# Performance work log

Hardware: AMD Instinct MI355X
Metric: run time of the kernel (lower is better)

Reference implementation:

```python
import jax, jax.numpy as jnp
import numpy as np

M = 12          # persons per frame
K = 2           # partition channels from conv1da (1024 = 2*512)
D = 512         # GCN channel dim / LSTM hidden
C_IN = 4096     # backbone feature dim
NUM_CLASSES = 8


def setup_inputs() -> dict:
    key = jax.random.key(0)
    ks = jax.random.split(key, 8)
    N, T = 16, 32
    NT = N * T
    base_out = jax.random.normal(ks[0], (NT, M, C_IN), dtype=jnp.float32)
    dist = jax.random.uniform(ks[1], (N, T, 3, K, M, M), dtype=jnp.float32)
    # conv1da: Conv1d(4096 -> 1024, k=1, bias=False) == matmul with [1024, 4096]
    w_a = jax.random.normal(ks[2], (K * D, C_IN), dtype=jnp.float32) * 0.02
    # LSTM(512, 512, 1): torch gate order i, f, g, o
    s = 1.0 / np.sqrt(D)
    w_ih = jax.random.uniform(ks[3], (4 * D, D), minval=-s, maxval=s, dtype=jnp.float32)
    w_hh = jax.random.uniform(ks[4], (4 * D, D), minval=-s, maxval=s, dtype=jnp.float32)
    b_ih = jax.random.uniform(ks[5], (4 * D,), minval=-s, maxval=s, dtype=jnp.float32)
    b_hh = jax.random.uniform(ks[6], (4 * D,), minval=-s, maxval=s, dtype=jnp.float32)
    # gclassifier: Linear(512 -> num_classes)
    w_cls = jax.random.normal(ks[7], (NUM_CLASSES, D), dtype=jnp.float32) * 0.01
    b_cls = jnp.zeros((NUM_CLASSES,), dtype=jnp.float32)
    return {"base_out": base_out, "dist": dist, "w_a": w_a,
            "w_ih": w_ih, "w_hh": w_hh, "b_ih": b_ih, "b_hh": b_hh,
            "w_cls": w_cls, "b_cls": b_cls, "n_videos": N}


def reference(base_out, dist, w_a, w_ih, w_hh, b_ih, b_hh, w_cls, b_cls, n_videos):
    NT = base_out.shape[0]
    N = n_videos
    T = NT // N
    # conv1da (1x1 conv, no bias): [NT, M, 4096] -> [NT, K*D, M] -> [NT, K, D, M]
    node1 = jnp.einsum('nmc,oc->nom', base_out, w_a).reshape(NT, K, D, M)
    # fused three-way adjacency aggregation: node1a + node1b + node1c
    A = (dist[:, :, 2] + dist[:, :, 1] + dist[:, :, 0]).reshape(NT, K, M, M)
    node = jnp.einsum('nkcv,nkvw->ncw', node1, A)  # [NT, D, M]
    node = jax.nn.relu(node)
    # AdaptiveAvgPool1d(1) over the M persons
    pooled = node.mean(axis=2)                      # [NT, D]
    seq = pooled.reshape(N, T, D)
    # torch nn.LSTM default batch_first=False: iterates over axis 0 (N), batch=T
    def step(carry, x_t):
        h, c = carry
        g = x_t @ w_ih.T + b_ih + h @ w_hh.T + b_hh  # [T, 4D]
        i, f, gg, o = jnp.split(g, 4, axis=-1)
        c = jax.nn.sigmoid(f) * c + jax.nn.sigmoid(i) * jnp.tanh(gg)
        h = jax.nn.sigmoid(o) * jnp.tanh(c)
        return (h, c), h
    h0 = jnp.zeros((T, D), dtype=seq.dtype)
    c0 = jnp.zeros((T, D), dtype=seq.dtype)
    _, hs = jax.lax.scan(step, (h0, c0), seq)       # [N, T, D]
    last = hs[:, -1, :]                              # video_feat[:, -1, :]
    return last @ w_cls.T + b_cls                    # [N, num_classes]
```

## Files before the change

### kernel.cpp

```cpp
#include <hip/hip_runtime.h>
#include <math.h>

#define MM 12
#define KK 2
#define DD 512
#define CIN 4096
#define NCLS 8
#define NV 16
#define TT 32

typedef unsigned long long u64;
typedef __attribute__((ext_vector_type(8))) __bf16 bf16x8;
typedef __attribute__((ext_vector_type(4))) float f32x4;

#define PART_F   0
#define POOLED_F 786432
#define TAGA_F   794624
#define TAGB_F   794880
#define PART_KS_STRIDE (192 * 1024)

#define MFMA_BF16(A, B, C) __builtin_amdgcn_mfma_f32_16x16x32_bf16((A), (B), (C), 0, 0, 0)

__global__ __launch_bounds__(256, 1) void k_fused(
    const float* __restrict__ base_out, const float* __restrict__ dist,
    const float* __restrict__ w_a, const float* __restrict__ w_ih,
    const float* __restrict__ w_hh, const float* __restrict__ b_ih,
    const float* __restrict__ b_hh, const float* __restrict__ w_cls,
    const float* __restrict__ b_cls,
    float* __restrict__ part, float* __restrict__ pooled,
    unsigned* __restrict__ tagA, unsigned* __restrict__ tagB,
    u64* __restrict__ slots, float* __restrict__ out)
{
  const int wg = blockIdx.x;
  const int tid = threadIdx.x;

  __shared__ __align__(16) unsigned short Ah[16 * 40], Al[16 * 40];
  __shared__ __align__(16) unsigned short Bh[192 * 40], Bl[192 * 40];
  __shared__ __align__(16) float whh_s[16][516];
  __shared__ __align__(16) float wih_s[16][516];
  __shared__ __align__(16) float pooled_s[16][520];
  __shared__ float gx_s[16][20];
  __shared__ __align__(16) float h_s[DD];
  __shared__ float dot_s[16];
  __shared__ float Asum_s[KK * MM * MM];

  {
    const int ks = wg >> 6, ot = wg & 63;
    const int cc0 = ks * 1024;
    const int wave = tid >> 6, lane = tid & 63;
    const int jf0 = wave * 3;

    const int sq = tid & 7;
    const int sr = tid >> 3;
    unsigned boff[6];
#pragma unroll
    for (int rep = 0; rep < 6; ++rep) {
      const int j = sr + 32 * rep;
      const int n = j / 12, m = j - n * 12;
      boff[rep] = (unsigned)(((n * TT + 31) * MM + m) * CIN + cc0 + sq * 4);
    }
    const bool aact = tid < 128;
    unsigned aoff = aact ? (unsigned)((ot * 16 + (tid >> 3)) * CIN + cc0 + sq * 4) : 0u;

    f32x4 acc0 = {0.f, 0.f, 0.f, 0.f}, acc1 = acc0, acc2 = acc0;

    float4 pa, pb[6];
    if (aact) pa = *(const float4*)&w_a[aoff];
#pragma unroll
    for (int rep = 0; rep < 6; ++rep) pb[rep] = *(const float4*)&base_out[boff[rep]];

    for (int st = 0; st < 32; ++st) {
      __syncthreads();
      if (aact) {
        const int idx = (tid >> 3) * 40 + sq * 4;
        unsigned ux = __float_as_uint(pa.x), uy = __float_as_uint(pa.y);
        unsigned uz = __float_as_uint(pa.z), uw = __float_as_uint(pa.w);
        *(uint2*)&Ah[idx] = make_uint2((ux >> 16) | (uy & 0xFFFF0000u),
                                       (uz >> 16) | (uw & 0xFFFF0000u));
        unsigned lx = __float_as_uint(pa.x - __uint_as_float(ux & 0xFFFF0000u));
        unsigned ly = __float_as_uint(pa.y - __uint_as_float(uy & 0xFFFF0000u));
        unsigned lz = __float_as_uint(pa.z - __uint_as_float(uz & 0xFFFF0000u));
        unsigned lw = __float_as_uint(pa.w - __uint_as_float(uw & 0xFFFF0000u));
        *(uint2*)&Al[idx] = make_uint2((lx >> 16) | (ly & 0xFFFF0000u),
                                       (lz >> 16) | (lw & 0xFFFF0000u));
      }
#pragma unroll
      for (int rep = 0; rep < 6; ++rep) {
        const int idx = (sr + 32 * rep) * 40 + sq * 4;
        unsigned ux = __float_as_uint(pb[rep].x), uy = __float_as_uint(pb[rep].y);
        unsigned uz = __float_as_uint(pb[rep].z), uw = __float_as_uint(pb[rep].w);
        *(uint2*)&Bh[idx] = make_uint2((ux >> 16) | (uy & 0xFFFF0000u),
                                       (uz >> 16) | (uw & 0xFFFF0000u));
        unsigned lx = __float_as_uint(pb[rep].x - __uint_as_float(ux & 0xFFFF0000u));
        unsigned ly = __float_as_uint(pb[rep].y - __uint_as_float(uy & 0xFFFF0000u));
        unsigned lz = __float_as_uint(pb[rep].z - __uint_as_float(uz & 0xFFFF0000u));
        unsigned lw = __float_as_uint(pb[rep].w - __uint_as_float(uw & 0xFFFF0000u));
        *(uint2*)&Bl[idx] = make_uint2((lx >> 16) | (ly & 0xFFFF0000u),
                                       (lz >> 16) | (lw & 0xFFFF0000u));
      }
      __syncthreads();
      if (st < 31) {
        aoff += 32;
        if (aact) pa = *(const float4*)&w_a[aoff];
#pragma unroll
        for (int rep = 0; rep < 6; ++rep) {
          boff[rep] += 32;
          pb[rep] = *(const float4*)&base_out[boff[rep]];
        }
      }
      const int koff = (lane >> 4) * 8;
      const int fra = (lane & 15) * 40 + koff;
      bf16x8 oh = *(const bf16x8*)&Ah[fra];
      bf16x8 ol = *(const bf16x8*)&Al[fra];
      {
        const int r0 = ((jf0 + 0) * 16 + (lane & 15)) * 40 + koff;
        bf16x8 jh = *(const bf16x8*)&Bh[r0], jl = *(const bf16x8*)&Bl[r0];
        acc0 = MFMA_BF16(jh, oh, acc0);
        acc0 = MFMA_BF16(jh, ol, acc0);
        acc0 = MFMA_BF16(jl, oh, acc0);
      }
      {
        const int r1 = ((jf0 + 1) * 16 + (lane & 15)) * 40 + koff;
        bf16x8 jh = *(const bf16x8*)&Bh[r1], jl = *(const bf16x8*)&Bl[r1];
        acc1 = MFMA_BF16(jh, oh, acc1);
        acc1 = MFMA_BF16(jh, ol, acc1);
        acc1 = MFMA_BF16(jl, oh, acc1);
      }
      {
        const int r2 = ((jf0 + 2) * 16 + (lane & 15)) * 40 + koff;
        bf16x8 jh = *(const bf16x8*)&Bh[r2], jl = *(const bf16x8*)&Bl[r2];
        acc2 = MFMA_BF16(jh, oh, acc2);
        acc2 = MFMA_BF16(jh, ol, acc2);
        acc2 = MFMA_BF16(jl, oh, acc2);
      }
    }
    const int o = ot * 16 + (lane & 15);
    const int jr = (lane >> 4) * 4;
#pragma unroll
    for (int r = 0; r < 4; ++r) {
      part[((size_t)ks * 192 + (jf0 + 0) * 16 + jr + r) * 1024 + o] = acc0[r];
      part[((size_t)ks * 192 + (jf0 + 1) * 16 + jr + r) * 1024 + o] = acc1[r];
      part[((size_t)ks * 192 + (jf0 + 2) * 16 + jr + r) * 1024 + o] = acc2[r];
    }
    __syncthreads();
    if (tid == 0)
      __hip_atomic_store(&tagA[wg], 1u, __ATOMIC_RELEASE, __HIP_MEMORY_SCOPE_AGENT);
  }

  if (wg < 128) {
    for (int f = tid; f < 16 * DD; f += 256) {
      const int rl = f >> 9, col = f & 511;
      const int row = (rl >> 2) * DD + wg * 4 + (rl & 3);
      whh_s[rl][col] = w_hh[(size_t)row * DD + col];
      wih_s[rl][col] = w_ih[(size_t)row * DD + col];
    }
  }

  while (__hip_atomic_load(&tagA[tid], __ATOMIC_RELAXED, __HIP_MEMORY_SCOPE_AGENT) != 1u) {}
  __syncthreads();
  (void)__hip_atomic_load(&tagA[0], __ATOMIC_ACQUIRE, __HIP_MEMORY_SCOPE_AGENT);

  {
    const int n = wg >> 4, cb = (wg & 15) * 32;
    const unsigned dbase = (unsigned)((n * TT + 31) * (3 * KK * MM * MM));
    for (int f = tid; f < KK * MM * MM; f += 256)
      Asum_s[f] = dist[dbase + f] + dist[dbase + KK * MM * MM + f]
                + dist[dbase + 2 * KK * MM * MM + f];
    __syncthreads();
    if (tid < 32) {
      const int c = cb + tid;
      float nd[KK][MM];
#pragma unroll
      for (int k = 0; k < KK; ++k)
#pragma unroll
        for (int v = 0; v < MM; ++v) {
          const size_t off = (size_t)(n * MM + v) * 1024 + k * DD + c;
          nd[k][v] = part[off] + part[off + PART_KS_STRIDE]
                   + part[off + 2 * PART_KS_STRIDE] + part[off + 3 * PART_KS_STRIDE];
        }
      float accm = 0.f;
#pragma unroll
      for (int w = 0; w < MM; ++w) {
        float sw = 0.f;
#pragma unroll
        for (int k = 0; k < KK; ++k)
#pragma unroll
          for (int v = 0; v < MM; ++v) sw += nd[k][v] * Asum_s[(k * MM + v) * MM + w];
        accm += fmaxf(sw, 0.f);
      }
      pooled[n * DD + c] = accm * (1.f / 12.f);
    }
    __syncthreads();
    if (tid == 0)
      __hip_atomic_store(&tagB[wg], 1u, __ATOMIC_RELEASE, __HIP_MEMORY_SCOPE_AGENT);
  }
  if (wg >= 128) return;

  while (__hip_atomic_load(&tagB[tid], __ATOMIC_RELAXED, __HIP_MEMORY_SCOPE_AGENT) != 1u) {}
  __syncthreads();
  (void)__hip_atomic_load(&tagB[0], __ATOMIC_ACQUIRE, __HIP_MEMORY_SCOPE_AGENT);

  for (int f = tid; f < NV * DD; f += 256) pooled_s[f >> 9][f & 511] = pooled[f];
  __syncthreads();
  {
    const int rl = tid & 15, n = tid >> 4;
    const float4* wr = (const float4*)&wih_s[rl][0];
    const float4* pv = (const float4*)&pooled_s[n][0];
    float a = 0.f;
#pragma unroll 8
    for (int q = 0; q < DD / 4; ++q) {
      float4 x = wr[q], y = pv[q];
      a += x.x * y.x + x.y * y.y + x.z * y.z + x.w * y.w;
    }
    const int row = (rl >> 2) * DD + wg * 4 + (rl & 3);
    gx_s[n][rl] = a + b_ih[row] + b_hh[row];
  }
  __syncthreads();

  {
    float c_reg = 0.f;
    const int r = tid >> 4;
    const int lj = tid & 15;

    for (int s = 0; s < NV; ++s) {
      if (s == 0) {
        h_s[tid] = 0.f; h_s[tid + 256] = 0.f;
      } else {
        const u64* slot = slots + ((size_t)(wg & 7) * NV + (s - 1)) * DD;
        u64 v0 = __hip_atomic_load(&slot[tid], __ATOMIC_RELAXED, __HIP_MEMORY_SCOPE_AGENT);
        u64 v1 = __hip_atomic_load(&slot[tid + 256], __ATOMIC_RELAXED, __HIP_MEMORY_SCOPE_AGENT);
        while ((unsigned)v0 != (unsigned)s)
          v0 = __hip_atomic_load(&slot[tid], __ATOMIC_RELAXED, __HIP_MEMORY_SCOPE_AGENT);
        while ((unsigned)v1 != (unsigned)s)
          v1 = __hip_atomic_load(&slot[tid + 256], __ATOMIC_RELAXED, __HIP_MEMORY_SCOPE_AGENT);
        h_s[tid] = __uint_as_float((unsigned)(v0 >> 32));
        h_s[tid + 256] = __uint_as_float((unsigned)(v1 >> 32));
      }
      __syncthreads();

      float p = 0.f;
      const float4* wrow = (const float4*)&whh_s[r][0];
      const float4* hv4 = (const float4*)h_s;
#pragma unroll
      for (int q = 0; q < 8; ++q) {
        float4 wv = wrow[lj + 16 * q];
        float4 hv = hv4[lj + 16 * q];
        p += wv.x * hv.x + wv.y * hv.y + wv.z * hv.z + wv.w * hv.w;
      }
#pragma unroll
      for (int off = 8; off; off >>= 1) p += __shfl_down(p, off, 16);
      if (lj == 0) dot_s[r] = p;
      __syncthreads();

      u64 pack = 0;
      if (tid < 4) {
        const float pi = gx_s[s][tid]      + dot_s[tid];
        const float pf = gx_s[s][4 + tid]  + dot_s[4 + tid];
        const float pg = gx_s[s][8 + tid]  + dot_s[8 + tid];
        const float po = gx_s[s][12 + tid] + dot_s[12 + tid];
        const float si = 1.f / (1.f + expf(-pi));
        const float sf = 1.f / (1.f + expf(-pf));
        const float so = 1.f / (1.f + expf(-po));
        c_reg = sf * c_reg + si * tanhf(pg);
        const float hn = so * tanhf(c_reg);
        pack = ((u64)__float_as_uint(hn) << 32) | (u64)(unsigned)(s + 1);
      }
      if (tid < 32) {
        u64 pk = __shfl(pack, tid & 3, 64);
        const int rep = tid >> 2;
        __hip_atomic_store(&slots[((size_t)rep * NV + s) * DD + wg * 4 + (tid & 3)], pk,
                           __ATOMIC_RELAXED, __HIP_MEMORY_SCOPE_AGENT);
      }
    }
  }

  if (wg == 0) {
    __syncthreads();
    for (int f = tid; f < NV * DD; f += 256) {
      const int ss = f >> 9, d = f & 511;
      u64 v = __hip_atomic_load(&slots[(size_t)ss * DD + d],
                                __ATOMIC_RELAXED, __HIP_MEMORY_SCOPE_AGENT);
      while ((unsigned)v != (unsigned)(ss + 1))
        v = __hip_atomic_load(&slots[(size_t)ss * DD + d],
                              __ATOMIC_RELAXED, __HIP_MEMORY_SCOPE_AGENT);
      pooled_s[ss][d] = __uint_as_float((unsigned)(v >> 32));
    }
    __syncthreads();
    if (tid < NV * NCLS) {
      const int n = tid >> 3, cl = tid & 7;
      const float4* hv = (const float4*)&pooled_s[n][0];
      const float4* wv = (const float4*)(w_cls + (size_t)cl * DD);
      float a = b_cls[cl];
#pragma unroll 8
      for (int q = 0; q < DD / 4; ++q) {
        float4 x = hv[q], y = wv[q];
        a += x.x * y.x + x.y * y.y + x.z * y.z + x.w * y.w;
      }
      out[tid] = a;
    }
  }
}

extern "C" void kernel_launch(void* const* d_in, const int* in_sizes, int n_in,
                              void* d_out, int out_size, void* d_ws, size_t ws_size,
                              hipStream_t stream) {
  const float* base_out = (const float*)d_in[0];
  const float* dist     = (const float*)d_in[1];
  const float* w_a      = (const float*)d_in[2];
  const float* w_ih     = (const float*)d_in[3];
  const float* w_hh     = (const float*)d_in[4];
  const float* b_ih     = (const float*)d_in[5];
  const float* b_hh     = (const float*)d_in[6];
  const float* w_cls    = (const float*)d_in[7];
  const float* b_cls    = (const float*)d_in[8];
  float* out = (float*)d_out;

  float* ws = (float*)d_ws;
  float* part   = ws + PART_F;
  float* pooled = ws + POOLED_F;
  unsigned* tagA = (unsigned*)(ws + TAGA_F);
  unsigned* tagB = (unsigned*)(ws + TAGB_F);
  u64* slots = (u64*)ws;

  k_fused<<<dim3(256), 256, 0, stream>>>(base_out, dist, w_a, w_ih, w_hh,
                                         b_ih, b_hh, w_cls, b_cls,
                                         part, pooled, tagA, tagB, slots, out);
}
```

Before: 277.2 us.

## Rework inter-block barriers with padded flags and per-step LSTM tag counters

Pads the grid-barrier flags to one per 64-byte line and polls them with a single wave using __all, so 256 threads no longer spin on flags that share cache lines. Replaces the 8-way replicated hidden-state slots with one global h buffer plus a per-workgroup step tag. Consumers first wait on the 128 tags and then read h. The final classifier gather batches its loads. The aim is lower polling traffic and cross-block sync latency in the sequential LSTM recurrence, at the cost of an extra tag wait per step and a loss of the replicated read locality.

```diff
diff --git a/kernel.cpp b/kernel.cpp
--- a/kernel.cpp
+++ b/kernel.cpp
@@ -16,10 +16,16 @@
 #define PART_F   0
 #define POOLED_F 786432
 #define TAGA_F   794624
-#define TAGB_F   794880
+#define TAGB_F   798720
+#define TAGD_F   802816
+#define HGLOB_F  804864
 #define PART_KS_STRIDE (192 * 1024)
 
 #define MFMA_BF16(A, B, C) __builtin_amdgcn_mfma_f32_16x16x32_bf16((A), (B), (C), 0, 0, 0)
+#define LOADR(p)      __hip_atomic_load((p), __ATOMIC_RELAXED, __HIP_MEMORY_SCOPE_AGENT)
+#define LOADACQ(p)    __hip_atomic_load((p), __ATOMIC_ACQUIRE, __HIP_MEMORY_SCOPE_AGENT)
+#define STORER(p, v)  __hip_atomic_store((p), (v), __ATOMIC_RELAXED, __HIP_MEMORY_SCOPE_AGENT)
+#define STOREREL(p, v) __hip_atomic_store((p), (v), __ATOMIC_RELEASE, __HIP_MEMORY_SCOPE_AGENT)
 
 __global__ __launch_bounds__(256, 1) void k_fused(
     const float* __restrict__ base_out, const float* __restrict__ dist,
@@ -29,7 +35,8 @@
     const float* __restrict__ b_cls,
     float* __restrict__ part, float* __restrict__ pooled,
     unsigned* __restrict__ tagA, unsigned* __restrict__ tagB,
-    u64* __restrict__ slots, float* __restrict__ out)
+    unsigned* __restrict__ tagD, u64* __restrict__ hg64,
+    float* __restrict__ out)
 {
   const int wg = blockIdx.x;
   const int tid = threadIdx.x;
@@ -143,8 +150,7 @@
       part[((size_t)ks * 192 + (jf0 + 2) * 16 + jr + r) * 1024 + o] = acc2[r];
     }
     __syncthreads();
-    if (tid == 0)
-      __hip_atomic_store(&tagA[wg], 1u, __ATOMIC_RELEASE, __HIP_MEMORY_SCOPE_AGENT);
+    if (tid == 0) STOREREL(&tagA[wg * 16], 1u);
   }
 
   if (wg < 128) {
@@ -156,9 +162,18 @@
     }
   }
 
-  while (__hip_atomic_load(&tagA[tid], __ATOMIC_RELAXED, __HIP_MEMORY_SCOPE_AGENT) != 1u) {}
+  if (tid < 64) {
+    bool done;
+    do {
+      unsigned a0 = LOADR(&tagA[(tid      ) * 16]);
+      unsigned a1 = LOADR(&tagA[(tid +  64) * 16]);
+      unsigned a2 = LOADR(&tagA[(tid + 128) * 16]);
+      unsigned a3 = LOADR(&tagA[(tid + 192) * 16]);
+      done = __all(a0 == 1u && a1 == 1u && a2 == 1u && a3 == 1u);
+    } while (!done);
+  }
   __syncthreads();
-  (void)__hip_atomic_load(&tagA[0], __ATOMIC_ACQUIRE, __HIP_MEMORY_SCOPE_AGENT);
+  (void)LOADACQ(&tagA[0]);
 
   {
     const int n = wg >> 4, cb = (wg & 15) * 32;
@@ -191,14 +206,22 @@
       pooled[n * DD + c] = accm * (1.f / 12.f);
     }
     __syncthreads();
-    if (tid == 0)
-      __hip_atomic_store(&tagB[wg], 1u, __ATOMIC_RELEASE, __HIP_MEMORY_SCOPE_AGENT);
+    if (tid == 0) STOREREL(&tagB[wg * 16], 1u);
   }
   if (wg >= 128) return;
 
-  while (__hip_atomic_load(&tagB[tid], __ATOMIC_RELAXED, __HIP_MEMORY_SCOPE_AGENT) != 1u) {}
+  if (tid < 64) {
+    bool done;
+    do {
+      unsigned a0 = LOADR(&tagB[(tid      ) * 16]);
+      unsigned a1 = LOADR(&tagB[(tid +  64) * 16]);
+      unsigned a2 = LOADR(&tagB[(tid + 128) * 16]);
+      unsigned a3 = LOADR(&tagB[(tid + 192) * 16]);
+      done = __all(a0 == 1u && a1 == 1u && a2 == 1u && a3 == 1u);
+    } while (!done);
+  }
   __syncthreads();
-  (void)__hip_atomic_load(&tagB[0], __ATOMIC_ACQUIRE, __HIP_MEMORY_SCOPE_AGENT);
+  (void)LOADACQ(&tagB[0]);
 
   for (int f = tid; f < NV * DD; f += 256) pooled_s[f >> 9][f & 511] = pooled[f];
   __syncthreads();
@@ -226,15 +249,22 @@
       if (s == 0) {
         h_s[tid] = 0.f; h_s[tid + 256] = 0.f;
       } else {
-        const u64* slot = slots + ((size_t)(wg & 7) * NV + (s - 1)) * DD;
-        u64 v0 = __hip_atomic_load(&slot[tid], __ATOMIC_RELAXED, __HIP_MEMORY_SCOPE_AGENT);
-        u64 v1 = __hip_atomic_load(&slot[tid + 256], __ATOMIC_RELAXED, __HIP_MEMORY_SCOPE_AGENT);
-        while ((unsigned)v0 != (unsigned)s)
-          v0 = __hip_atomic_load(&slot[tid], __ATOMIC_RELAXED, __HIP_MEMORY_SCOPE_AGENT);
-        while ((unsigned)v1 != (unsigned)s)
-          v1 = __hip_atomic_load(&slot[tid + 256], __ATOMIC_RELAXED, __HIP_MEMORY_SCOPE_AGENT);
-        h_s[tid] = __uint_as_float((unsigned)(v0 >> 32));
-        h_s[tid + 256] = __uint_as_float((unsigned)(v1 >> 32));
+        if (tid < 64) {
+          bool done;
+          do {
+            int t0 = (int)LOADR(&tagD[(tid     ) * 16]);
+            int t1 = (int)LOADR(&tagD[(tid + 64) * 16]);
+            done = __all(t0 >= s && t1 >= s);
+          } while (!done);
+        }
+        __syncthreads();
+        const size_t hb = (size_t)(s - 1) * 512 + 2 * tid;
+        u64 v0 = LOADR(&hg64[hb]);
+        u64 v1 = LOADR(&hg64[hb + 1]);
+        while ((unsigned)v0 != (unsigned)s) v0 = LOADR(&hg64[hb]);
+        while ((unsigned)v1 != (unsigned)s) v1 = LOADR(&hg64[hb + 1]);
+        *(float2*)&h_s[2 * tid] = make_float2(__uint_as_float((unsigned)(v0 >> 32)),
+                                              __uint_as_float((unsigned)(v1 >> 32)));
       }
       __syncthreads();
 
@@ -252,7 +282,6 @@
       if (lj == 0) dot_s[r] = p;
       __syncthreads();
 
-      u64 pack = 0;
       if (tid < 4) {
         const float pi = gx_s[s][tid]      + dot_s[tid];
         const float pf = gx_s[s][4 + tid]  + dot_s[4 + tid];
@@ -263,27 +292,32 @@
         const float so = 1.f / (1.f + expf(-po));
         c_reg = sf * c_reg + si * tanhf(pg);
         const float hn = so * tanhf(c_reg);
-        pack = ((u64)__float_as_uint(hn) << 32) | (u64)(unsigned)(s + 1);
-      }
-      if (tid < 32) {
-        u64 pk = __shfl(pack, tid & 3, 64);
-        const int rep = tid >> 2;
-        __hip_atomic_store(&slots[((size_t)rep * NV + s) * DD + wg * 4 + (tid & 3)], pk,
-                           __ATOMIC_RELAXED, __HIP_MEMORY_SCOPE_AGENT);
-      }
+        const u64 pk = ((u64)__float_as_uint(hn) << 32) | (u64)(unsigned)(s + 1);
+        STORER(&hg64[(size_t)s * 512 + wg * 4 + tid], pk);
+      }
+      if (tid == 0) STORER(&tagD[wg * 16], (unsigned)(s + 1));
     }
   }
 
   if (wg == 0) {
-    __syncthreads();
-    for (int f = tid; f < NV * DD; f += 256) {
-      const int ss = f >> 9, d = f & 511;
-      u64 v = __hip_atomic_load(&slots[(size_t)ss * DD + d],
-                                __ATOMIC_RELAXED, __HIP_MEMORY_SCOPE_AGENT);
-      while ((unsigned)v != (unsigned)(ss + 1))
-        v = __hip_atomic_load(&slots[(size_t)ss * DD + d],
-                              __ATOMIC_RELAXED, __HIP_MEMORY_SCOPE_AGENT);
-      pooled_s[ss][d] = __uint_as_float((unsigned)(v >> 32));
+    if (tid < 64) {
+      bool done;
+      do {
+        int t0 = (int)LOADR(&tagD[(tid     ) * 16]);
+        int t1 = (int)LOADR(&tagD[(tid + 64) * 16]);
+        done = __all(t0 >= NV && t1 >= NV);
+      } while (!done);
+    }
+    __syncthreads();
+    u64 vv[32];
+#pragma unroll
+    for (int q = 0; q < 32; ++q) vv[q] = LOADR(&hg64[tid + 256 * q]);
+#pragma unroll
+    for (int q = 0; q < 32; ++q) {
+      const int f = tid + 256 * q;
+      u64 v = vv[q];
+      while ((unsigned)v != (unsigned)((f >> 9) + 1)) v = LOADR(&hg64[f]);
+      pooled_s[f >> 9][f & 511] = __uint_as_float((unsigned)(v >> 32));
     }
     __syncthreads();
     if (tid < NV * NCLS) {
@@ -320,9 +354,10 @@
   float* pooled = ws + POOLED_F;
   unsigned* tagA = (unsigned*)(ws + TAGA_F);
   unsigned* tagB = (unsigned*)(ws + TAGB_F);
-  u64* slots = (u64*)ws;
+  unsigned* tagD = (unsigned*)(ws + TAGD_F);
+  u64* hg64 = (u64*)(ws + HGLOB_F);
 
   k_fused<<<dim3(256), 256, 0, stream>>>(base_out, dist, w_a, w_ih, w_hh,
                                          b_ih, b_hh, w_cls, b_cls,
-                                         part, pooled, tagA, tagB, slots, out);
+                                         part, pooled, tagA, tagB, tagD, hg64, out);
 }
```

After: 274.2 us. No clear change (-1.1%).
